# Kernel optimization log

Hardware: AMD Instinct MI355X
Metric: run time of the kernel (lower is better)

## Reference

```python
import jax, jax.numpy as jnp
import numpy as np

K = 3           # kernel_size
N_LAYERS = 2    # n_layers; circuit applies StronglyEntanglingLayers(weights) N_LAYERS times
STRIDE = 2
N_QUBITS = K * K  # 9 qubits -> 512-dim statevector


def _apply_1q(state, U, q):
    """Apply 2x2 unitary U (shared (2,2) or per-batch (P,2,2)) to qubit q.
    state: (P,) + (2,)*N_QUBITS complex64."""
    s = jnp.moveaxis(state, 1 + q, -1)
    if U.ndim == 3:
        s = jnp.einsum('pji,p...i->p...j', U, s)
    else:
        s = jnp.einsum('ji,...i->...j', U, s)
    return jnp.moveaxis(s, -1, 1 + q)


def _apply_cnot(state, c, t):
    """CNOT with control c, target t on state (P,)+(2,)*n."""
    s0 = jnp.take(state, 0, axis=1 + c)
    s1 = jnp.take(state, 1, axis=1 + c)
    t_ax = 1 + t if t < c else t  # target axis after control axis removed
    s1 = jnp.flip(s1, axis=t_ax)
    return jnp.stack([s0, s1], axis=1 + c)


def _rot_matrix(phi, theta, omega):
    """PennyLane Rot(phi, theta, omega) = RZ(omega) RY(theta) RZ(phi)."""
    c = jnp.cos(theta / 2)
    s = jnp.sin(theta / 2)
    u00 = jnp.exp(-0.5j * (phi + omega)) * c
    u01 = -jnp.exp(0.5j * (phi - omega)) * s
    u10 = jnp.exp(-0.5j * (phi - omega)) * s
    u11 = jnp.exp(0.5j * (phi + omega)) * c
    return jnp.stack([jnp.stack([u00, u01]), jnp.stack([u10, u11])]).astype(jnp.complex64)


def _circuit(angles, weights):
    """angles: (P, N_QUBITS) float32. Returns PauliZ expvals (P, N_QUBITS) float32."""
    P = angles.shape[0]
    n = N_QUBITS
    state = jnp.zeros((P, 2 ** n), jnp.complex64).at[:, 0].set(1.0)
    state = state.reshape((P,) + (2,) * n)
    # AngleEmbedding (default rotation = RX) per wire, angle varies per patch
    half = angles / 2
    cos = jnp.cos(half)
    sin = jnp.sin(half)
    for q in range(n):
        c = cos[:, q].astype(jnp.complex64)
        s = (-1j * sin[:, q]).astype(jnp.complex64)
        U = jnp.stack([jnp.stack([c, s], -1), jnp.stack([s, c], -1)], -2)  # (P,2,2)
        state = _apply_1q(state, U, q)
    # Faithful to source: StronglyEntanglingLayers(weights) applied N_LAYERS times,
    # each containing N_LAYERS internal layers (Rot on each wire + CNOT ring).
    for _ in range(N_LAYERS):
        for l in range(N_LAYERS):
            for q in range(n):
                state = _apply_1q(
                    state,
                    _rot_matrix(weights[l, q, 0], weights[l, q, 1], weights[l, q, 2]),
                    q,
                )
            r = (l % (n - 1)) + 1  # PennyLane default ranges
            for q in range(n):
                state = _apply_cnot(state, q, (q + r) % n)
    probs = state.real ** 2 + state.imag ** 2  # (P,)+(2,)*n
    exps = []
    for q in range(n):
        axes = tuple(ax for ax in range(1, n + 1) if ax != 1 + q)
        m = probs.sum(axis=axes)  # (P, 2)
        exps.append(m[:, 0] - m[:, 1])
    return jnp.stack(exps, axis=1)


def _forward(input, weights):
    B, _, H, W = input.shape
    out = (H - K) // STRIDE + 1
    starts = jnp.arange(out) * STRIDE
    win = starts[:, None] + jnp.arange(K)  # (out, K) row/col start offsets
    x = input[:, 0]  # (B, H, W), channels asserted == 1
    # vectorized sliding-window patch extraction: (B, out, out, K, K)
    patches = x[:, win[:, None, :, None], win[None, :, None, :]]
    angles = patches.reshape(B * out * out, N_QUBITS)  # row-major flatten, matches torch.flatten
    ev = _circuit(angles, weights)  # (B*out*out, N_QUBITS)
    ev = ev.reshape(B, out * out, N_QUBITS).transpose(0, 2, 1)
    return ev.reshape(B, N_QUBITS, out, out).astype(jnp.float32)


def setup_inputs() -> dict:
    key = jax.random.key(0)
    k1, k2 = jax.random.split(key)
    inp = jax.random.normal(k1, (8, 1, 128, 128), dtype=jnp.float32)
    weights = jax.random.uniform(k2, (N_LAYERS, N_QUBITS, 3), dtype=jnp.float32,
                                 minval=0.0, maxval=2 * np.pi)
    return {"input": inp, "weights": weights}


def reference(input, weights):
    return _forward(input, weights)
```

## Files before the change

kernel.cpp:

```cpp
#include <hip/hip_runtime.h>
#include <hip/hip_fp16.h>


namespace {

constexpr int OUT_HW = 63;
constexpr int N_PIX = OUT_HW * OUT_HW;
constexpr int PPB = 4;
constexpr int N_PATCH_TOTAL = 8 * N_PIX;

typedef _Float16 h2 __attribute__((ext_vector_type(2)));
typedef __fp16  hw2 __attribute__((ext_vector_type(2)));

__device__ __forceinline__ int h2i(h2 v) { return __builtin_bit_cast(int, v); }
__device__ __forceinline__ h2  i2h(int v) { return __builtin_bit_cast(h2, v); }
__device__ __forceinline__ h2  swap_h2(h2 v) { return __builtin_shufflevector(v, v, 1, 0); }

__device__ __forceinline__ h2 pk_mul(h2 x, h2 y) {
    return __builtin_bit_cast(h2, __hmul2(__builtin_bit_cast(__half2, x),
                                          __builtin_bit_cast(__half2, y)));
}
__device__ __forceinline__ h2 pk_fma(h2 x, h2 y, h2 z) {
    return __builtin_bit_cast(h2, __hfma2(__builtin_bit_cast(__half2, x),
                                          __builtin_bit_cast(__half2, y),
                                          __builtin_bit_cast(__half2, z)));
}

__device__ __forceinline__ int bperm_i(int addr, int v) {
    return __builtin_amdgcn_ds_bpermute(addr, v);
}

template<int M>
__device__ __forceinline__ int shfl_i(int v, int lane) {
    if constexpr (M == 1) {
        return __builtin_amdgcn_mov_dpp(v, 0xB1, 0xF, 0xF, false);
    } else if constexpr (M == 2) {
        return __builtin_amdgcn_mov_dpp(v, 0x4E, 0xF, 0xF, false);
    } else if constexpr (M == 8) {
        return __builtin_amdgcn_mov_dpp(v, 0x128, 0xF, 0xF, false);
    } else if constexpr (M < 32) {
        return __builtin_amdgcn_ds_swizzle(v, 0x1F | (M << 10));
    } else {
        return bperm_i((lane << 2) ^ 128, v);
    }
}
template<int M>
__device__ __forceinline__ float shfl_f(float v, int lane) {
    return __int_as_float(shfl_i<M>(__float_as_int(v), lane));
}

template<int C, int T>
__device__ __forceinline__ void cnot16(h2 (&a)[16])
{
    constexpr int cm = 1 << C, tm = 1 << T;
    #pragma unroll
    for (int r = 0; r < 16; ++r) {
        if ((r & cm) && !(r & tm)) {
            const int r1 = r | tm;
            const h2 t = a[r]; a[r] = a[r1]; a[r1] = t;
        }
    }
}

__device__ __forceinline__ void ring1_partial16(h2 (&a)[16], int lane)
{
    cnot16<0,1>(a);
    cnot16<1,2>(a);
    cnot16<2,3>(a);
    const int l5 = lane & 31;
    const int hi = (lane & 32) << 2;
    const int sA = ((l5 ^ ((l5 & 15) << 1)) << 2) | hi;
    const int sB = sA ^ 4;
    #pragma unroll
    for (int r = 0; r < 16; ++r)
        a[r] = i2h(bperm_i((r & 8) ? sB : sA, h2i(a[r])));
}

__device__ __forceinline__ void ring2_partial16(h2 (&a)[16], int lane)
{
    cnot16<0,2>(a);
    cnot16<1,3>(a);
    const int l5 = lane & 31;
    const int s0 = ((l5 ^ ((l5 & 7) << 2)) << 2) | ((lane & 32) << 2);
    #pragma unroll
    for (int r = 0; r < 16; ++r) {
        const int ad = s0 ^ (((r >> 3) & 1) << 3) ^ (((r >> 2) & 1) << 2);
        a[r] = i2h(bperm_i(ad, h2i(a[r])));
    }
}

__device__ __forceinline__ void load_diag16(h2 (&cc)[16], h2 (&ns)[16],
                                            const int* __restrict__ dtab,
                                            int dbase, int lane5)
{
    #pragma unroll
    for (int r = 0; r < 16; ++r) {
        const int idx = (dbase + r * 32 + lane5) * 2;
        cc[r] = i2h(dtab[idx]);
        ns[r] = i2h(dtab[idx + 1]);
    }
}

__device__ __forceinline__ void apply_diag16_pre(h2 (&a)[16],
                                                 const h2 (&cc)[16],
                                                 const h2 (&ns)[16])
{
    #pragma unroll
    for (int r = 0; r < 16; ++r)
        a[r] = pk_fma(ns[r], swap_h2(a[r]), pk_mul(cc[r], a[r]));
}

template<int QM>
__device__ __forceinline__ void regY16(h2 (&a)[16], h2 A2, h2 B2, h2 C2, h2 D2)
{
    #pragma unroll
    for (int r = 0; r < 16; ++r) {
        if (!(r & QM)) {
            const int r1 = r | QM;
            const h2 x0 = a[r], x1 = a[r1];
            a[r]  = pk_fma(B2, x1, pk_mul(A2, x0));
            a[r1] = pk_fma(D2, x1, pk_mul(C2, x0));
        }
    }
}

template<int LM>
__device__ __forceinline__ void laneY16(h2 (&a)[16], int lane, h2 c2, h2 sp2)
{
    #pragma unroll
    for (int r = 0; r < 16; ++r) {
        const h2 p = i2h(shfl_i<LM>(h2i(a[r]), lane));
        a[r] = pk_fma(sp2, p, pk_mul(c2, a[r]));
    }
}

__device__ __forceinline__ void apply_Y16(h2 (&a)[16], int lane,
                                          const int* __restrict__ yt,
                                          bool sw0, bool sw1)
{
    {   const int cc = yt[0], ss = yt[1], ns = yt[2];
        regY16<1>(a, i2h(sw0 ? ns : cc), i2h(sw0 ? cc : ns),
                     i2h(sw0 ? cc : ss), i2h(sw0 ? ss : cc)); }
    {   const int cc = yt[3], ss = yt[4], ns = yt[5];
        regY16<2>(a, i2h(sw1 ? ns : cc), i2h(sw1 ? cc : ns),
                     i2h(sw1 ? cc : ss), i2h(sw1 ? ss : cc)); }
    {   regY16<4>(a, i2h(yt[6]),  i2h(yt[8]),  i2h(yt[7]),  i2h(yt[6])); }
    {   regY16<8>(a, i2h(yt[9]),  i2h(yt[11]), i2h(yt[10]), i2h(yt[9])); }
    {   laneY16<1> (a, lane, i2h(yt[12]), i2h((lane & 1)        ? yt[13] : yt[14])); }
    {   laneY16<2> (a, lane, i2h(yt[15]), i2h(((lane >> 1) & 1) ? yt[16] : yt[17])); }
    {   laneY16<4> (a, lane, i2h(yt[18]), i2h(((lane >> 2) & 1) ? yt[19] : yt[20])); }
    {   laneY16<8> (a, lane, i2h(yt[21]), i2h(((lane >> 3) & 1) ? yt[22] : yt[23])); }
    {   laneY16<16>(a, lane, i2h(yt[24]), i2h(((lane >> 4) & 1) ? yt[25] : yt[26])); }
}

__global__ void precomp_kernel(const float* __restrict__ w, float* __restrict__ ws)
{
    const int tid = threadIdx.x;
    float* rot = ws;
    int* ytab = (int*)(ws + 144);
    int* dtab = (int*)(ws + 208);
    if (tid < 18) {
        const float phi = w[tid*3 + 0], theta = w[tid*3 + 1], omega = w[tid*3 + 2];
        const float ct = cosf(0.5f * theta), st = sinf(0.5f * theta);
        const float apo = 0.5f * (phi + omega), amo = 0.5f * (phi - omega);
        const float ca = cosf(apo), sa = sinf(apo);
        const float cm = cosf(amo), sm = sinf(amo);
        float* m = rot + tid * 8;
        m[0] =  ca * ct; m[1] = -sa * ct;
        m[2] = -cm * st; m[3] = -sm * st;
        m[4] =  cm * st; m[5] = -sm * st;
        m[6] =  ca * ct; m[7] =  sa * ct;
        h2 cc; cc.x = (_Float16)ct;  cc.y = (_Float16)ct;
        h2 ss; ss.x = (_Float16)st;  ss.y = (_Float16)st;
        h2 ns; ns.x = (_Float16)(-st); ns.y = (_Float16)(-st);
        ytab[tid*3 + 0] = h2i(cc);
        ytab[tid*3 + 1] = h2i(ss);
        ytab[tid*3 + 2] = h2i(ns);
    }
    if (tid < 192) {
        const int vmask[9] = {0x1FE,0x003,0x007,0x00F,0x01F,0x03F,0x07F,0x0FF,0x1FF};
        const int wmask[9] = {0x0AB,0x157,0x005,0x00A,0x015,0x02A,0x055,0x0AA,0x155};
        const int d = tid >> 6, ln = tid & 63;
        for (int r = 0; r < 8; ++r) {
            const int p = (ln << 3) | r;
            float ang = 0.f;
            for (int q = 0; q < 9; ++q) {
                if (d == 0) {
                    const float lam = -0.5f * w[(9 + q)*3 + 0];
                    ang += (__popc(p & vmask[q]) & 1) ? -lam : lam;
                } else if (d == 1) {
                    const float lam = -0.5f * w[q*3 + 0];
                    ang += (__popc(p & wmask[q]) & 1) ? -lam : lam;
                    const float lm2 = -0.5f * w[(9 + q)*3 + 2];
                    ang += ((p >> q) & 1) ? -lm2 : lm2;
                } else {
                    const float lam = -0.5f * w[(9 + q)*3 + 0];
                    ang += (__popc(p & vmask[q]) & 1) ? -lam : lam;
                    const float lm2 = -0.5f * w[q*3 + 2];
                    ang += ((p >> q) & 1) ? -lm2 : lm2;
                }
            }
            const float c = cosf(ang), s = sinf(ang);
            h2 cc;  cc.x = (_Float16)c;    cc.y = (_Float16)c;
            h2 nsp; nsp.x = (_Float16)(-s); nsp.y = (_Float16)s;
            const int idx = (d * 512 + (p & 15) * 32 + (p >> 4)) * 2;
            dtab[idx + 0] = h2i(cc);
            dtab[idx + 1] = h2i(nsp);
        }
    }
}

__global__ __launch_bounds__(PPB * 64, 6) void qconv_kernel(
    const float* __restrict__ x,
    const float* __restrict__ ws,
    float* __restrict__ out)
{
    const float* rot  = ws;
    const int* ytab = (const int*)(ws + 144);
    const int* dtab = (const int*)(ws + 208);

    const int lane   = threadIdx.x & 63;
    const int wv     = threadIdx.x >> 6;
    const int lane5  = lane & 31;
    const int half   = lane >> 5;
    const int patch2 = (blockIdx.x * PPB + wv) * 2;

    __shared__ __align__(16) float abtab[PPB][2][36];
    {
        auto stage_val = [&](int h, int j) {
            const int q = j >> 2, comp = j & 3;
            const int tp   = patch2 + h;
            const int tb   = tp / N_PIX;
            const int trem = tp - tb * N_PIX;
            const int toy  = trem / OUT_HW;
            const int tox  = trem - toy * OUT_HW;
            const int qr = q / 3, qc = q - 3 * qr;
            const float ang = x[tb * 16384 + (toy * 2 + qr) * 128 + (tox * 2 + qc)];
            float s, c;
            __sincosf(0.5f * ang, &s, &c);
            const float* R = rot + 8 * q;
            float v;
            if      (comp == 0) v = c*R[0] + s*R[3];
            else if (comp == 1) v = c*R[1] - s*R[2];
            else if (comp == 2) v = c*R[4] + s*R[7];
            else                v = c*R[5] - s*R[6];
            abtab[wv][h][j] = v;
        };
        const int h1 = (lane >= 36) ? 1 : 0;
        stage_val(h1, lane - 36 * h1);
        if (lane < 8) stage_val(1, 28 + lane);
    }
    __builtin_amdgcn_wave_barrier();

    float ab[36];
    {
        const float4* src = reinterpret_cast<const float4*>(&abtab[wv][half][0]);
        float4* dst = reinterpret_cast<float4*>(ab);
        #pragma unroll
        for (int j = 0; j < 9; ++j) dst[j] = src[j];
    }

    h2 dcc[16], dns[16];
    load_diag16(dcc, dns, dtab, 0 * 512, lane5);

    h2 a[16];
    {
        const int bit0 = lane5 & 1;
        float Lr = bit0 ? ab[18] : ab[16];
        float Li = bit0 ? ab[19] : ab[17];
        #pragma unroll
        for (int q = 5; q <= 8; ++q) {
            const int bit = (lane5 >> (q - 4)) & 1;
            const float fr = bit ? ab[4*q + 2] : ab[4*q + 0];
            const float fi = bit ? ab[4*q + 3] : ab[4*q + 1];
            const float nr = Lr*fr - Li*fi;
            const float ni = Lr*fi + Li*fr;
            Lr = nr; Li = ni;
        }
        float c01r[4], c01i[4], c23r[4], c23i[4];
        #pragma unroll
        for (int j = 0; j < 4; ++j) {
            const float f0r = (j & 1) ? ab[2]  : ab[0];
            const float f0i = (j & 1) ? ab[3]  : ab[1];
            const float f1r = (j & 2) ? ab[6]  : ab[4];
            const float f1i = (j & 2) ? ab[7]  : ab[5];
            c01r[j] = f0r*f1r - f0i*f1i;
            c01i[j] = f0r*f1i + f0i*f1r;
            const float g2r = (j & 1) ? ab[10] : ab[8];
            const float g2i = (j & 1) ? ab[11] : ab[9];
            const float g3r = (j & 2) ? ab[14] : ab[12];
            const float g3i = (j & 2) ? ab[15] : ab[13];
            c23r[j] = g2r*g3r - g2i*g3i;
            c23i[j] = g2r*g3i + g2i*g3r;
        }
        float hlr[4], hli[4];
        #pragma unroll
        for (int j = 0; j < 4; ++j) {
            hlr[j] = c01r[j]*Lr - c01i[j]*Li;
            hli[j] = c01r[j]*Li + c01i[j]*Lr;
        }
        #pragma unroll
        for (int r = 0; r < 16; ++r) {
            const float fr = hlr[r & 3]*c23r[r >> 2] - hli[r & 3]*c23i[r >> 2];
            const float fi = hlr[r & 3]*c23i[r >> 2] + hli[r & 3]*c23r[r >> 2];
            a[r] = __builtin_bit_cast(h2, __builtin_amdgcn_cvt_pkrtz(fr, fi));
        }
    }

    const bool q7b = ((lane >> 3) & 1) != 0;
    const bool q8b = ((lane >> 4) & 1) != 0;

    apply_diag16_pre(a, dcc, dns);
    load_diag16(dcc, dns, dtab, 1 * 512, lane5);
    ring1_partial16(a, lane);
    apply_Y16(a, lane, ytab + 27, q8b, false);
    apply_diag16_pre(a, dcc, dns);
    load_diag16(dcc, dns, dtab, 2 * 512, lane5);
    ring2_partial16(a, lane);
    apply_Y16(a, lane, ytab + 0, q7b, q8b);
    apply_diag16_pre(a, dcc, dns);
    ring1_partial16(a, lane);
    apply_Y16(a, lane, ytab + 27, q8b, false);

    float p[16];
    #pragma unroll
    for (int r = 0; r < 16; ++r) {
#if __has_builtin(__builtin_amdgcn_fdot2)
        p[r] = __builtin_amdgcn_fdot2(__builtin_bit_cast(hw2, a[r]),
                                      __builtin_bit_cast(hw2, a[r]), 0.0f, false);
#else
        const float xr = (float)a[r].x, xi = (float)a[r].y;
        p[r] = xr*xr + xi*xi;
#endif
    }

    float A[8], B[8];
    #pragma unroll
    for (int j = 0; j < 8; ++j) {
        A[j] = p[2*j] + p[2*j+1];
        B[j] = p[2*j] - p[2*j+1];
    }
    float P5[4], P7[4], P10[4];
    #pragma unroll
    for (int k = 0; k < 4; ++k) {
        P5[k]  = B[2*k] + B[2*k+1];
        P7[k]  = B[2*k] - B[2*k+1];
        P10[k] = A[2*k] - A[2*k+1];
    }
    float S5  = (P5[0]  - P5[1])  + (P5[2]  - P5[3]);
    float S7  = (P7[0]  - P7[1])  + (P7[2]  - P7[3]);
    float S11 = (P7[0]  + P7[1])  - (P7[2]  + P7[3]);
    float S10 = (P10[0] + P10[1]) - (P10[2] + P10[3]);

    const int sm0 = (lane & 1) << 31;
    const int sm1 = ((lane >> 1) & 1) << 31;
    const int sm2 = ((lane >> 2) & 1) << 31;
    const int sm3 = ((lane >> 3) & 1) << 31;
    const int sm4 = ((lane >> 4) & 1) << 31;
#define WHT_STAGE(M, SM) { \
    const float qa = shfl_f<M>(S5, lane),  qb = shfl_f<M>(S7, lane); \
    const float qc = shfl_f<M>(S10, lane), qd = shfl_f<M>(S11, lane); \
    S5  = qa + __int_as_float(__float_as_int(S5)  ^ (SM)); \
    S7  = qb + __int_as_float(__float_as_int(S7)  ^ (SM)); \
    S10 = qc + __int_as_float(__float_as_int(S10) ^ (SM)); \
    S11 = qd + __int_as_float(__float_as_int(S11) ^ (SM)); }
    WHT_STAGE(1,  sm0)
    WHT_STAGE(2,  sm1)
    WHT_STAGE(4,  sm2)
    WHT_STAGE(8,  sm3)
    WHT_STAGE(16, sm4)
#undef WHT_STAGE

    const int patch = patch2 + half;
    const int b   = patch / N_PIX;
    const int rem = patch - b * N_PIX;
    const int oy  = rem / OUT_HW;
    const int ox  = rem - oy * OUT_HW;
    const int base = b * 9;
    const int pix  = oy * OUT_HW + ox;

    if (lane5 == 0x00) {
        out[(base + 2) * N_PIX + pix] = S5;
        out[(base + 3) * N_PIX + pix] = S10;
    }
    if (lane5 == 0x01) out[(base + 4) * N_PIX + pix] = S5;
    if (lane5 == 0x02) out[(base + 5) * N_PIX + pix] = S10;
    if (lane5 == 0x05) out[(base + 6) * N_PIX + pix] = S5;
    if (lane5 == 0x0A) {
        out[(base + 7) * N_PIX + pix] = S10;
        out[(base + 0) * N_PIX + pix] = S11;
    }
    if (lane5 == 0x15) {
        out[(base + 8) * N_PIX + pix] = S5;
        out[(base + 1) * N_PIX + pix] = S7;
    }
}

}

extern "C" void kernel_launch(void* const* d_in, const int* in_sizes, int n_in,
                              void* d_out, int out_size, void* d_ws, size_t ws_size,
                              hipStream_t stream)
{
    const float* x = (const float*)d_in[0];
    const float* w = (const float*)d_in[1];
    float* ws = (float*)d_ws;
    float* out = (float*)d_out;

    precomp_kernel<<<1, 256, 0, stream>>>(w, ws);
    qconv_kernel<<<N_PATCH_TOTAL / (PPB * 2), PPB * 64, 0, stream>>>(x, ws, out);
}
```

Measured before the change: 109.8 us.

## Stage diagonal phase table in LDS and raise occupancy target

Each block now copies the 3x512 diagonal-phase table from global memory into shared memory once, and each diagonal step reads its coefficients from LDS on the fly. This replaces the prefetch of 32 packed registers per diagonal, freeing registers so the launch bound can go from 6 to 8 waves per SIMD. In exchange it adds a 12 KB LDS copy per block, a full __syncthreads in place of a wave barrier, and exposed LDS latency on the diagonal steps, and the LDS footprint may itself limit occupancy.

```diff
diff --git a/kernel.cpp b/kernel.cpp
--- a/kernel.cpp
+++ b/kernel.cpp
@@ -89,25 +89,16 @@
     }
 }
 
-__device__ __forceinline__ void load_diag16(h2 (&cc)[16], h2 (&ns)[16],
-                                            const int* __restrict__ dtab,
-                                            int dbase, int lane5)
-{
-    #pragma unroll
-    for (int r = 0; r < 16; ++r) {
-        const int idx = (dbase + r * 32 + lane5) * 2;
-        cc[r] = i2h(dtab[idx]);
-        ns[r] = i2h(dtab[idx + 1]);
-    }
-}
-
-__device__ __forceinline__ void apply_diag16_pre(h2 (&a)[16],
-                                                 const h2 (&cc)[16],
-                                                 const h2 (&ns)[16])
-{
-    #pragma unroll
-    for (int r = 0; r < 16; ++r)
-        a[r] = pk_fma(ns[r], swap_h2(a[r]), pk_mul(cc[r], a[r]));
+__device__ __forceinline__ void apply_diag16_lds(h2 (&a)[16],
+                                                 const int* __restrict__ dlds,
+                                                 int dbase, int lane5)
+{
+    #pragma unroll
+    for (int r = 0; r < 16; ++r) {
+        const int2 v = *reinterpret_cast<const int2*>(
+                           &dlds[(dbase + r * 32 + lane5) * 2]);
+        a[r] = pk_fma(i2h(v.y), swap_h2(a[r]), pk_mul(i2h(v.x), a[r]));
+    }
 }
 
 template<int QM>
@@ -210,7 +201,7 @@
     }
 }
 
-__global__ __launch_bounds__(PPB * 64, 6) void qconv_kernel(
+__global__ __launch_bounds__(PPB * 64, 8) void qconv_kernel(
     const float* __restrict__ x,
     const float* __restrict__ ws,
     float* __restrict__ out)
@@ -225,7 +216,18 @@
     const int half   = lane >> 5;
     const int patch2 = (blockIdx.x * PPB + wv) * 2;
 
+    __shared__ __align__(16) int   dlds[3 * 512 * 2];
     __shared__ __align__(16) float abtab[PPB][2][36];
+
+    {
+        const int t = threadIdx.x;
+        const int4* src = reinterpret_cast<const int4*>(dtab);
+        int4* dst = reinterpret_cast<int4*>(dlds);
+        #pragma unroll
+        for (int k = 0; k < 3; ++k)
+            dst[t + 256 * k] = src[t + 256 * k];
+    }
+
     {
         auto stage_val = [&](int h, int j) {
             const int q = j >> 2, comp = j & 3;
@@ -250,7 +252,7 @@
         stage_val(h1, lane - 36 * h1);
         if (lane < 8) stage_val(1, 28 + lane);
     }
-    __builtin_amdgcn_wave_barrier();
+    __syncthreads();
 
     float ab[36];
     {
@@ -259,9 +261,6 @@
         #pragma unroll
         for (int j = 0; j < 9; ++j) dst[j] = src[j];
     }
-
-    h2 dcc[16], dns[16];
-    load_diag16(dcc, dns, dtab, 0 * 512, lane5);
 
     h2 a[16];
     {
@@ -310,15 +309,13 @@
     const bool q7b = ((lane >> 3) & 1) != 0;
     const bool q8b = ((lane >> 4) & 1) != 0;
 
-    apply_diag16_pre(a, dcc, dns);
-    load_diag16(dcc, dns, dtab, 1 * 512, lane5);
+    apply_diag16_lds(a, dlds, 0 * 512, lane5);
     ring1_partial16(a, lane);
     apply_Y16(a, lane, ytab + 27, q8b, false);
-    apply_diag16_pre(a, dcc, dns);
-    load_diag16(dcc, dns, dtab, 2 * 512, lane5);
+    apply_diag16_lds(a, dlds, 1 * 512, lane5);
     ring2_partial16(a, lane);
     apply_Y16(a, lane, ytab + 0, q7b, q8b);
-    apply_diag16_pre(a, dcc, dns);
+    apply_diag16_lds(a, dlds, 2 * 512, lane5);
     ring1_partial16(a, lane);
     apply_Y16(a, lane, ytab + 27, q8b, false);
 
```

New measurement: 109.0 us. No clear change (-0.7%).
